# Optimization experiments

Hardware: AMD Instinct MI355X
Metric: run time of the kernel (lower is better)

Reference implementation:

```python
import jax, jax.numpy as jnp
import numpy as np

B, S, HID = 2, 2048, 2304
H, KVH, D = 8, 4, 256          # query heads, kv heads, head_dim
N_REP = H // KVH
SCALE = 256.0 ** -0.5          # query_pre_attn_scalar ** -0.5
SOFTCAP = 50.0
ROPE_THETA = 10000.0
NEG = -1e9


def setup_inputs() -> dict:
    key = jax.random.key(0)
    k1, k2, k3, k4, k5 = jax.random.split(key, 5)
    hidden_states = jax.random.normal(k1, (B, S, HID), dtype=jnp.float32)
    # RoPE cos/sin tables, shape [B, S, D]
    inv_freq = 1.0 / (ROPE_THETA ** (jnp.arange(0, D, 2, dtype=jnp.float32) / D))
    pos = jnp.arange(S, dtype=jnp.float32)
    freqs = pos[:, None] * inv_freq[None, :]            # [S, D/2]
    emb = jnp.concatenate([freqs, freqs], axis=-1)      # [S, D]
    cos = jnp.broadcast_to(jnp.cos(emb)[None], (B, S, D))
    sin = jnp.broadcast_to(jnp.sin(emb)[None], (B, S, D))
    # additive causal mask [B, 1, S, S] (sliding_window=4096 > S, so pure causal)
    idx = jnp.arange(S)
    causal = idx[None, :] <= idx[:, None]
    attention_mask = jnp.broadcast_to(
        jnp.where(causal, 0.0, NEG).astype(jnp.float32)[None, None], (B, 1, S, S))
    # projection weights (lecun-normal-ish scale), no bias (attention_bias=False)
    Wq = jax.random.normal(k2, (HID, H * D), dtype=jnp.float32) / np.sqrt(HID)
    Wk = jax.random.normal(k3, (HID, KVH * D), dtype=jnp.float32) / np.sqrt(HID)
    Wv = jax.random.normal(k4, (HID, KVH * D), dtype=jnp.float32) / np.sqrt(HID)
    Wo = jax.random.normal(k5, (H * D, HID), dtype=jnp.float32) / np.sqrt(H * D)
    return {"hidden_states": hidden_states, "cos": cos, "sin": sin,
            "attention_mask": attention_mask,
            "Wq": Wq, "Wk": Wk, "Wv": Wv, "Wo": Wo}


def _rotate_half(x):
    half = x.shape[-1] // 2
    return jnp.concatenate([-x[..., half:], x[..., :half]], axis=-1)


def reference(hidden_states, cos, sin, attention_mask, Wq, Wk, Wv, Wo):
    b, s, _ = hidden_states.shape
    q = (hidden_states @ Wq).reshape(b, s, H, D).transpose(0, 2, 1, 3)    # [B,H,S,D]
    k = (hidden_states @ Wk).reshape(b, s, KVH, D).transpose(0, 2, 1, 3)  # [B,KVH,S,D]
    v = (hidden_states @ Wv).reshape(b, s, KVH, D).transpose(0, 2, 1, 3)
    c = cos[:, None]  # [B,1,S,D] broadcast over heads (unsqueeze_dim=1)
    sn = sin[:, None]
    q = q * c + _rotate_half(q) * sn
    k = k * c + _rotate_half(k) * sn
    # GQA: repeat kv heads (interleave, matching repeat_kv tile+reshape)
    k = jnp.repeat(k, N_REP, axis=1)
    v = jnp.repeat(v, N_REP, axis=1)
    w = jnp.einsum('bhqd,bhkd->bhqk', q, k) * SCALE
    w = jnp.tanh(w / SOFTCAP) * SOFTCAP                  # logit softcapping
    w = w + attention_mask[:, :, :, :s]
    w = jax.nn.softmax(w.astype(jnp.float32), axis=-1).astype(q.dtype)
    out = jnp.einsum('bhqk,bhkd->bhqd', w, v)
    out = out.transpose(0, 2, 1, 3).reshape(b, s, H * D)
    return out @ Wo
```

## Files before the change

kernel.cpp:

```cpp
#include <hip/hip_runtime.h>

typedef unsigned short u16;
typedef __attribute__((ext_vector_type(8))) short short8;
typedef __attribute__((ext_vector_type(4))) float f32x4;
typedef __attribute__((ext_vector_type(4))) unsigned short us4;

constexpr int B_ = 2;
constexpr int H_ = 8;
constexpr int KVH_ = 4;
constexpr int S_ = 2048;
constexpr int D_ = 256;
constexpr int HID_ = 2304;
constexpr int QKVN_ = 4096;
constexpr int AON_ = 2048;

__device__ __forceinline__ float b2f(u16 u) {
  union { float f; unsigned int i; } x; x.i = ((unsigned int)u) << 16; return x.f;
}
__device__ __forceinline__ u16 f2b(float f) {
  unsigned int x = __float_as_uint(f);
  unsigned int r = (x + 0x7fffu + ((x >> 16) & 1u)) >> 16;
  return (u16)r;
}
__device__ __forceinline__ float exp2_raw(float x) {
  float r;
  asm("v_exp_f32 %0, %1" : "=v"(r) : "v"(x));
  return r;
}
__device__ __forceinline__ unsigned int cvt_pk_bf16(float lo, float hi) {
  unsigned int r;
  asm("v_cvt_pk_bf16_f32 %0, %1, %2" : "=v"(r) : "v"(lo), "v"(hi));
  return r;
}

__global__ void cast_kernel(const float* __restrict__ in, u16* __restrict__ out) {
  size_t i = ((size_t)blockIdx.x * 256 + threadIdx.x) * 4;
  float4 v = *(const float4*)(in + i);
  unsigned int lo = (unsigned int)f2b(v.x) | ((unsigned int)f2b(v.y) << 16);
  unsigned int hi = (unsigned int)f2b(v.z) | ((unsigned int)f2b(v.w) << 16);
  uint2 o; o.x = lo; o.y = hi;
  *(uint2*)(out + i) = o;
}

__global__ void transpose_cast_all(const float* __restrict__ s0, const float* __restrict__ s1,
                                   const float* __restrict__ s2, const float* __restrict__ s3,
                                   u16* __restrict__ d0, u16* __restrict__ d1,
                                   u16* __restrict__ d2, u16* __restrict__ d3) {
  __shared__ float tile[64][65];
  int which = blockIdx.z;
  const float* src; u16* dst; int R, C;
  if (which == 0)      { src = s0; dst = d0; R = 2304; C = 2048; }
  else if (which == 1) { src = s1; dst = d1; R = 2304; C = 1024; }
  else if (which == 2) { src = s2; dst = d2; R = 2304; C = 1024; }
  else                 { src = s3; dst = d3; R = 2048; C = 2304; }
  int r0 = blockIdx.y * 64, c0 = blockIdx.x * 64;
  if (r0 >= R || c0 >= C) return;
  int t = threadIdx.x;
#pragma unroll
  for (int i = 0; i < 16; ++i) {
    int e = i * 256 + t;
    int r = e >> 6, c = e & 63;
    tile[r][c] = src[(size_t)(r0 + r) * C + (c0 + c)];
  }
  __syncthreads();
#pragma unroll
  for (int i = 0; i < 8; ++i) {
    int e = i * 256 + t;
    int orow = e >> 5;
    int ocol = (e & 31) * 2;
    unsigned int w = (unsigned int)f2b(tile[ocol][orow]) |
                     ((unsigned int)f2b(tile[ocol + 1][orow]) << 16);
    *(unsigned int*)(&dst[(size_t)(c0 + orow) * R + (r0 + ocol)]) = w;
  }
}

template <int OUTF32>
__global__ __launch_bounds__(512, 2) void gemm_bt8(
    const u16* __restrict__ A, const u16* __restrict__ B, void* __restrict__ Cp,
    int M, int N, int K) {
  __shared__ u16 lds[2][2][2][8192];
  const int tid = threadIdx.x;
  const int lane = tid & 63;
  const int wave = tid >> 6;
  const int wm = wave >> 2, wn = wave & 3;
  const int quad = lane >> 4, l16 = lane & 15;
  const int m0 = blockIdx.y * 256, n0 = blockIdx.x * 256;
  const int nt = K >> 6;

  const int sub = tid >> 6;
  const int rr = (tid >> 2) & 15;
  const int cc = ((tid & 3) * 8) ^ ((rr & 8) ? 16 : 0);
  const int r_rel = (sub >> 1) * 16 + rr;
  const int ccol = (sub & 1) * 32 + cc;
  const u16* Asrc = A + (size_t)(m0 + r_rel) * K + ccol;
  const u16* Bsrc = B + (size_t)(n0 + r_rel) * K + ccol;
  const int ldsc = tid * 8;

  const int fr_off = l16 * 64 + (((quad * 8) ^ ((l16 & 8) ? 16 : 0)) << 1);

#define GL8(src, dst)                                                                  \
  __builtin_amdgcn_global_load_lds((const __attribute__((address_space(1))) void*)(src), \
                                   (__attribute__((address_space(3))) void*)(dst), 16, 0, 0)
#define STAGE_A(bf, kt, qp) {                                                          \
    const u16* _s = Asrc + (size_t)(kt) * 64;                                          \
    GL8(_s + (size_t)((qp) * 64) * K,       &lds[bf][0][0][(qp) * 4096 + ldsc]);       \
    GL8(_s + (size_t)(128 + (qp) * 64) * K, &lds[bf][0][1][(qp) * 4096 + ldsc]); }
#define STAGE_B(bf, kt, hf) {                                                          \
    const u16* _s = Bsrc + (size_t)(kt) * 64;                                          \
    GL8(_s + (size_t)((hf) * 128) * K,      &lds[bf][1][hf][ldsc]);                    \
    GL8(_s + (size_t)((hf) * 128 + 64) * K, &lds[bf][1][hf][4096 + ldsc]); }
#define LDA(bf, mi, kk) \
  (*(const short8*)((const char*)&lds[bf][0][wm][0] + (mi) * 2048 + (kk) * 1024 + fr_off))
#define LDB(bf, ni, kk) \
  (*(const short8*)((const char*)&lds[bf][1][wn >> 1][0] + ((wn & 1) * 4 + (ni)) * 2048 + (kk) * 1024 + fr_off))

  f32x4 acc[8][4] = {};
  short8 bfr[4][2], af[2][2];

  STAGE_B(0, 0, 0); STAGE_B(0, 0, 1); STAGE_A(0, 0, 0); STAGE_A(0, 0, 1);
  STAGE_B(1, 1, 0); STAGE_B(1, 1, 1); STAGE_A(1, 1, 0);
  asm volatile("s_waitcnt vmcnt(6)" ::: "memory");
  __builtin_amdgcn_s_barrier();

#define PHASE(q, STG, VMW)                                                             \
    _Pragma("unroll") for (int i = 0; i < 2; ++i)                                      \
      _Pragma("unroll") for (int kk = 0; kk < 2; ++kk) af[i][kk] = LDA(c, 2 * (q) + i, kk); \
    STG; VMW;                                                                          \
    __builtin_amdgcn_s_barrier();                                                      \
    asm volatile("s_waitcnt lgkmcnt(0)" ::: "memory");                                 \
    __builtin_amdgcn_sched_barrier(0);                                                 \
    __builtin_amdgcn_s_setprio(1);                                                     \
    _Pragma("unroll") for (int i = 0; i < 2; ++i)                                      \
      _Pragma("unroll") for (int ni = 0; ni < 4; ++ni)                                 \
        _Pragma("unroll") for (int kk = 0; kk < 2; ++kk)                               \
          acc[2 * (q) + i][ni] = __builtin_amdgcn_mfma_f32_16x16x32_bf16(              \
              af[i][kk], bfr[ni][kk], acc[2 * (q) + i][ni], 0, 0, 0);                  \
    __builtin_amdgcn_s_setprio(0);                                                     \
    __builtin_amdgcn_s_barrier();

  for (int T = 0; T < nt; ++T) {
    const int c = T & 1;
#pragma unroll
    for (int ni = 0; ni < 4; ++ni)
#pragma unroll
      for (int kk = 0; kk < 2; ++kk) bfr[ni][kk] = LDB(c, ni, kk);
    PHASE(0, if (T + 1 < nt) STAGE_A(c ^ 1, T + 1, 1), )
    PHASE(1, if (T + 2 < nt) STAGE_B(c, T + 2, 0), )
    PHASE(2, if (T + 2 < nt) STAGE_B(c, T + 2, 1), )
    PHASE(3, if (T + 2 < nt) STAGE_A(c, T + 2, 0),
          if (T + 2 >= nt) { asm volatile("s_waitcnt vmcnt(0)" ::: "memory"); }
          else             { asm volatile("s_waitcnt vmcnt(6)" ::: "memory"); })
  }
#undef PHASE
#undef LDA
#undef LDB
#undef STAGE_A
#undef STAGE_B
#undef GL8

#pragma unroll
  for (int mi = 0; mi < 8; ++mi) {
#pragma unroll
    for (int ni = 0; ni < 4; ++ni) {
#pragma unroll
      for (int r = 0; r < 4; ++r) {
        int row = m0 + wm * 128 + mi * 16 + quad * 4 + r;
        int col = n0 + wn * 64 + ni * 16 + l16;
        if (OUTF32)
          ((float*)Cp)[(size_t)row * N + col] = acc[mi][ni][r];
        else
          ((u16*)Cp)[(size_t)row * N + col] = f2b(acc[mi][ni][r]);
      }
    }
  }
}

__global__ void rope_kernel(const u16* __restrict__ qkv, const float* __restrict__ cs,
                            const float* __restrict__ sn, u16* __restrict__ Qr,
                            u16* __restrict__ Kr) {
  int t = threadIdx.x;
  int row = blockIdx.x * 8 + (t >> 5);
  int d0 = (t & 31) * 4;
  int b = row >> 11, s = row & 2047;
  const u16* qrow = qkv + (size_t)row * QKVN_;
  float4 c4 = *(const float4*)(cs + (size_t)row * D_ + d0);
  float4 s4 = *(const float4*)(sn + (size_t)row * D_ + d0);
  float c[4] = {c4.x, c4.y, c4.z, c4.w};
  float sv[4] = {s4.x, s4.y, s4.z, s4.w};
#pragma unroll
  for (int h = 0; h < H_ + KVH_; ++h) {
    const u16* src = qrow + (h < H_ ? h * D_ : 2048 + (h - H_) * D_);
    us4 lo = *(const us4*)(src + d0);
    us4 hi = *(const us4*)(src + 128 + d0);
    us4 olo, ohi;
#pragma unroll
    for (int j = 0; j < 4; ++j) {
      float xl = b2f(lo[j]), xh = b2f(hi[j]);
      olo[j] = f2b(xl * c[j] - xh * sv[j]);
      ohi[j] = f2b(xh * c[j] + xl * sv[j]);
    }
    u16* dst = (h < H_)
        ? Qr + ((size_t)(b * H_ + h) * S_ + s) * D_
        : Kr + ((size_t)(b * KVH_ + (h - H_)) * S_ + s) * D_;
    *(us4*)(dst + d0) = olo;
    *(us4*)(dst + 128 + d0) = ohi;
  }
}

__global__ void transpose_v(const u16* __restrict__ qkv, u16* __restrict__ Vt) {
  __shared__ u16 tile[64][72];
  int d0 = blockIdx.x * 64, s0 = blockIdx.y * 64, g = blockIdx.z;
  int b = g >> 2, kvh = g & 3;
  int t = threadIdx.x;
#pragma unroll
  for (int i = 0; i < 8; ++i) {
    int e = i * 256 + t;
    int r = e >> 5, c = (e & 31) * 2;
    unsigned int v = *(const unsigned int*)(&qkv[(size_t)(b * S_ + s0 + r) * QKVN_ +
                                                 3072 + kvh * D_ + d0 + c]);
    tile[r][c] = (u16)v;
    tile[r][c + 1] = (u16)(v >> 16);
  }
  __syncthreads();
#pragma unroll
  for (int i = 0; i < 8; ++i) {
    int e = i * 256 + t;
    int orow = e >> 5, ocol = (e & 31) * 2;
    unsigned int w = (unsigned int)tile[ocol][orow] |
                     ((unsigned int)tile[ocol + 1][orow] << 16);
    *(unsigned int*)(&Vt[((size_t)g * D_ + d0 + orow) * S_ + s0 + ocol]) = w;
  }
}

__global__ __launch_bounds__(256, 2) void attn_kernel(
    const u16* __restrict__ Qr, const u16* __restrict__ Kr, const u16* __restrict__ Vt,
    float* __restrict__ Op0, float* __restrict__ Op1,
    float* __restrict__ Lp0, float* __restrict__ Lp1) {
  __shared__ u16 Ks[2][32 * 256];
  __shared__ u16 Vs[2][32 * 256];
  int bx = blockIdx.x;
  int h = bx & 7;
  int u = bx >> 4;
  int sp = (bx >> 3) & 1;
  int kvh = h >> 1;
  int tid = threadIdx.x, wave = tid >> 6, lane = tid & 63;
  int quad = lane >> 4, l16 = lane & 15;
  float* Op = sp ? Op1 : Op0;
  float* Lp = sp ? Lp1 : Lp0;
  int ksrc_s[4], ksrc_c[4], vsrc_d[4], vsrc_s[4];
#pragma unroll
  for (int i = 0; i < 4; ++i) {
    int p = i * 256 + tid;
    int sK = p >> 5;
    ksrc_s[i] = sK;
    ksrc_c[i] = (p & 31) ^ ((sK & 3) | (((sK >> 3) & 1) << 2));
    vsrc_d[i] = p >> 2;
    vsrc_s[i] = (p & 3) ^ ((p >> 3) & 3);
  }
  const int kg = l16 >> 2, ka = l16 & 3;
  const int srow0 = 8 * kg + ka;
  const int ksw = ka | ((kg & 1) << 2);

  for (int part = 0; part < 2; ++part) {
    int b = part;
    int qt = (part == 0) ? u : (31 - u);
    int q0 = qt * 64;
    int beg = sp ? (qt + 1) : 0;
    int end = sp ? (2 * qt + 2) : (qt + 1);
    const u16* Qbase = Qr + ((size_t)(b * H_ + h) * S_ + q0 + wave * 16 + l16) * D_;
    short8 qf[8];
#pragma unroll
    for (int kk = 0; kk < 8; ++kk)
      qf[kk] = *(const short8*)(Qbase + kk * 32 + quad * 8);
    const u16* Kbase = Kr + (size_t)(b * KVH_ + kvh) * S_ * D_;
    const u16* Vbase = Vt + (size_t)(b * KVH_ + kvh) * D_ * S_;
    float lp = 0.f;
    f32x4 o_acc[16] = {};
    const int qq = q0 + wave * 16 + l16;

#define STAGE(KT, BUF)                                                                   \
    {                                                                                    \
      int k0s = (KT) * 32;                                                               \
      _Pragma("unroll") for (int i = 0; i < 4; ++i) {                                    \
        int p = i * 256 + tid;                                                           \
        __builtin_amdgcn_global_load_lds(                                                \
            (const __attribute__((address_space(1))) void*)(Kbase +                      \
                (size_t)(k0s + ksrc_s[i]) * D_ + ksrc_c[i] * 8),                         \
            (__attribute__((address_space(3))) void*)(&Ks[BUF][0] + p * 8), 16, 0, 0);   \
      }                                                                                  \
      _Pragma("unroll") for (int i = 0; i < 4; ++i) {                                    \
        int p = i * 256 + tid;                                                           \
        __builtin_amdgcn_global_load_lds(                                                \
            (const __attribute__((address_space(1))) void*)(Vbase +                      \
                (size_t)vsrc_d[i] * S_ + k0s + vsrc_s[i] * 8),                           \
            (__attribute__((address_space(3))) void*)(&Vs[BUF][0] + p * 8), 16, 0, 0);   \
      }                                                                                  \
    }

    STAGE(beg, 0);
    __syncthreads();
    for (int kt = beg; kt < end; ++kt) {
      int k0 = kt * 32;
      int cur = (kt - beg) & 1;
      if (kt + 1 < end) STAGE(kt + 1, cur ^ 1);
      f32x4 sacc[2] = {};
      __builtin_amdgcn_s_setprio(1);
#pragma unroll
      for (int n = 0; n < 2; ++n) {
        const u16* kb = &Ks[cur][0] + (srow0 + 4 * n) * 256;
#pragma unroll
        for (int kk = 0; kk < 8; ++kk) {
          int phys = (kk * 4 + quad) ^ ksw;
          short8 kfr = *(const short8*)(kb + phys * 8);
          sacc[n] = __builtin_amdgcn_mfma_f32_16x16x32_bf16(kfr, qf[kk], sacc[n], 0, 0, 0);
        }
      }
      __builtin_amdgcn_s_setprio(0);
      bool full = (k0 + 31 <= q0 + wave * 16);
#pragma unroll
      for (int n = 0; n < 2; ++n) {
#pragma unroll
        for (int r = 0; r < 4; ++r) {
          float E = exp2_raw(sacc[n][r] * 0.0036067376f);
          float ee = exp2_raw(__frcp_rn(E + 1.0f) * -144.2695041f);
          if (!full) {
            int key = k0 + 8 * quad + 4 * n + r;
            ee = (key <= qq) ? ee : 0.0f;
          }
          lp += ee;
          sacc[n][r] = ee;
        }
      }
      union { short8 s8; unsigned int d[4]; } pu;
      pu.d[0] = cvt_pk_bf16(sacc[0][0], sacc[0][1]);
      pu.d[1] = cvt_pk_bf16(sacc[0][2], sacc[0][3]);
      pu.d[2] = cvt_pk_bf16(sacc[1][0], sacc[1][1]);
      pu.d[3] = cvt_pk_bf16(sacc[1][2], sacc[1][3]);
      short8 pa = pu.s8;
      __builtin_amdgcn_s_setprio(1);
#pragma unroll
      for (int dt = 0; dt < 16; ++dt) {
        int d = dt * 16 + l16;
        int phys = quad ^ ((d >> 1) & 3);
        short8 vb = *(const short8*)(&Vs[cur][0] + d * 32 + phys * 8);
        o_acc[dt] = __builtin_amdgcn_mfma_f32_16x16x32_bf16(pa, vb, o_acc[dt], 0, 0, 0);
      }
      __builtin_amdgcn_s_setprio(0);
      __syncthreads();
    }
#undef STAGE
    lp += __shfl_xor(lp, 16, 64);
    lp += __shfl_xor(lp, 32, 64);
    if (lane < 16)
      Lp[((size_t)(b * H_ + h)) * S_ + q0 + wave * 16 + lane] = lp;
#pragma unroll
    for (int dt = 0; dt < 16; ++dt)
#pragma unroll
      for (int r = 0; r < 4; ++r) {
        int row = b * S_ + q0 + wave * 16 + quad * 4 + r;
        int col = h * D_ + dt * 16 + l16;
        Op[(size_t)row * AON_ + col] = o_acc[dt][r];
      }
  }
}

__global__ void combine_kernel(const float* __restrict__ Op0, const float* __restrict__ Op1,
                               const float* __restrict__ Lp0, const float* __restrict__ Lp1,
                               u16* __restrict__ Ao) {
  size_t idx = (size_t)blockIdx.x * 256 + threadIdx.x;
  size_t row = idx >> 9;
  int c4 = ((int)idx & 511) * 4;
  const float4 a = *(const float4*)(Op0 + row * AON_ + c4);
  const float4 b4 = *(const float4*)(Op1 + row * AON_ + c4);
  int b = (int)(row >> 11), s = (int)row & 2047;
  int h = c4 >> 8;
  size_t li = ((size_t)(b * H_ + h)) * S_ + s;
  float inv = 1.0f / (Lp0[li] + Lp1[li]);
  unsigned int lo = (unsigned int)f2b((a.x + b4.x) * inv) | ((unsigned int)f2b((a.y + b4.y) * inv) << 16);
  unsigned int hi = (unsigned int)f2b((a.z + b4.z) * inv) | ((unsigned int)f2b((a.w + b4.w) * inv) << 16);
  uint2 o; o.x = lo; o.y = hi;
  *(uint2*)(Ao + row * AON_ + c4) = o;
}

extern "C" void kernel_launch(void* const* d_in, const int* in_sizes, int n_in,
                              void* d_out, int out_size, void* d_ws, size_t ws_size,
                              hipStream_t stream) {
  const float* hidden = (const float*)d_in[0];
  const float* cosp = (const float*)d_in[1];
  const float* sinp = (const float*)d_in[2];
  const float* Wq = (const float*)d_in[4];
  const float* Wk = (const float*)d_in[5];
  const float* Wv = (const float*)d_in[6];
  const float* Wo = (const float*)d_in[7];

  u16* hs  = (u16*)d_ws;
  u16* WT  = hs  + (size_t)4096 * HID_;
  u16* WoT = WT  + (size_t)4096 * HID_;
  u16* qkv = WoT + (size_t)HID_ * AON_;
  u16* Qr  = qkv + (size_t)4096 * QKVN_;
  u16* Kr  = Qr  + (size_t)B_ * H_ * S_ * D_;
  u16* Vt  = Kr  + (size_t)B_ * KVH_ * S_ * D_;
  u16* Ao  = Vt  + (size_t)B_ * KVH_ * S_ * D_;
  float* Lp0 = (float*)(Ao + (size_t)4096 * AON_);
  float* Lp1 = Lp0 + (size_t)B_ * H_ * S_;
  float* Op0 = (float*)hs;
  float* Op1 = (float*)qkv;

  cast_kernel<<<9216, 256, 0, stream>>>(hidden, hs);
  transpose_cast_all<<<dim3(36, 36, 4), 256, 0, stream>>>(
      Wq, Wk, Wv, Wo, WT, WT + (size_t)2048 * HID_, WT + (size_t)3072 * HID_, WoT);
  gemm_bt8<0><<<dim3(16, 16), 512, 0, stream>>>(hs, WT, qkv, 4096, QKVN_, HID_);
  rope_kernel<<<512, 256, 0, stream>>>(qkv, cosp, sinp, Qr, Kr);
  transpose_v<<<dim3(4, 32, 8), 256, 0, stream>>>(qkv, Vt);
  attn_kernel<<<dim3(512), 256, 0, stream>>>(Qr, Kr, Vt, Op0, Op1, Lp0, Lp1);
  combine_kernel<<<16384, 256, 0, stream>>>(Op0, Op1, Lp0, Lp1, Ao);
  gemm_bt8<1><<<dim3(9, 16), 512, 0, stream>>>(Ao, WoT, d_out, 4096, HID_, 2048);
}
```

Baseline: 397.7 us.

## Merge prep and rope/V-transpose launches; use smaller-tile GEMM for output projection

Folds the hidden-state cast and the four weight transpose-casts into one launch, with a flattened grid that no longer spawns idle blocks. RoPE and the V transpose are merged into a single kernel the same way, which removes two launches. The output projection moves from the 256x256-tile GEMM (144 blocks) to a new 128x128-tile GEMM using direct global-to-LDS loads (576 blocks) to fill more CUs. The cost is a simpler GEMM with no software pipelining and more blocks that each reread the shared inputs.

```diff
diff --git a/kernel.cpp b/kernel.cpp
--- a/kernel.cpp
+++ b/kernel.cpp
@@ -33,29 +33,31 @@
   return r;
 }
 
-__global__ void cast_kernel(const float* __restrict__ in, u16* __restrict__ out) {
-  size_t i = ((size_t)blockIdx.x * 256 + threadIdx.x) * 4;
-  float4 v = *(const float4*)(in + i);
-  unsigned int lo = (unsigned int)f2b(v.x) | ((unsigned int)f2b(v.y) << 16);
-  unsigned int hi = (unsigned int)f2b(v.z) | ((unsigned int)f2b(v.w) << 16);
-  uint2 o; o.x = lo; o.y = hi;
-  *(uint2*)(out + i) = o;
-}
-
-__global__ void transpose_cast_all(const float* __restrict__ s0, const float* __restrict__ s1,
-                                   const float* __restrict__ s2, const float* __restrict__ s3,
-                                   u16* __restrict__ d0, u16* __restrict__ d1,
-                                   u16* __restrict__ d2, u16* __restrict__ d3) {
+__global__ void prep_kernel(const float* __restrict__ hidden,
+                            const float* __restrict__ s0, const float* __restrict__ s1,
+                            const float* __restrict__ s2, const float* __restrict__ s3,
+                            u16* __restrict__ hsOut,
+                            u16* __restrict__ d0, u16* __restrict__ d1,
+                            u16* __restrict__ d2, u16* __restrict__ d3) {
   __shared__ float tile[64][65];
-  int which = blockIdx.z;
-  const float* src; u16* dst; int R, C;
-  if (which == 0)      { src = s0; dst = d0; R = 2304; C = 2048; }
-  else if (which == 1) { src = s1; dst = d1; R = 2304; C = 1024; }
-  else if (which == 2) { src = s2; dst = d2; R = 2304; C = 1024; }
-  else                 { src = s3; dst = d3; R = 2048; C = 2304; }
-  int r0 = blockIdx.y * 64, c0 = blockIdx.x * 64;
-  if (r0 >= R || c0 >= C) return;
+  int bx = blockIdx.x;
   int t = threadIdx.x;
+  if (bx < 9216) {
+    size_t i = ((size_t)bx * 256 + t) * 4;
+    float4 v = *(const float4*)(hidden + i);
+    unsigned int lo = (unsigned int)f2b(v.x) | ((unsigned int)f2b(v.y) << 16);
+    unsigned int hi = (unsigned int)f2b(v.z) | ((unsigned int)f2b(v.w) << 16);
+    uint2 o; o.x = lo; o.y = hi;
+    *(uint2*)(hsOut + i) = o;
+    return;
+  }
+  int tt = bx - 9216;
+  const float* src; u16* dst; int R, C, cx, cy;
+  if (tt < 1152)              { src = s0; dst = d0; R = 2304; C = 2048; cx = tt & 31; cy = tt >> 5; }
+  else if ((tt -= 1152) < 576){ src = s1; dst = d1; R = 2304; C = 1024; cx = tt & 15; cy = tt >> 4; }
+  else if ((tt -= 576) < 576) { src = s2; dst = d2; R = 2304; C = 1024; cx = tt & 15; cy = tt >> 4; }
+  else { tt -= 576;             src = s3; dst = d3; R = 2048; C = 2304; cx = tt % 36; cy = tt / 36; }
+  int r0 = cy * 64, c0 = cx * 64;
 #pragma unroll
   for (int i = 0; i < 16; ++i) {
     int e = i * 256 + t;
@@ -175,43 +177,108 @@
   }
 }
 
-__global__ void rope_kernel(const u16* __restrict__ qkv, const float* __restrict__ cs,
-                            const float* __restrict__ sn, u16* __restrict__ Qr,
-                            u16* __restrict__ Kr) {
+template <int OUTF32>
+__global__ __launch_bounds__(256, 2) void gemm_bt(
+    const u16* __restrict__ A, const u16* __restrict__ B, void* __restrict__ Cp,
+    int M, int N, int K) {
+  __shared__ u16 As[128 * 32];
+  __shared__ u16 Bs[128 * 32];
+  int m0 = blockIdx.y * 128, n0 = blockIdx.x * 128;
+  int tid = threadIdx.x;
+  int lane = tid & 63, wave = tid >> 6;
+  int wy = wave >> 1, wx = wave & 1;
+  int quad = lane >> 4, l16 = lane & 15;
+  f32x4 acc[4][4] = {};
+  for (int k0 = 0; k0 < K; k0 += 32) {
+#pragma unroll
+    for (int i = 0; i < 2; ++i) {
+      int chunk = i * 256 + tid;
+      int row = chunk >> 2, col = (chunk & 3) << 3;
+      __builtin_amdgcn_global_load_lds(
+          (const __attribute__((address_space(1))) void*)(A + (size_t)(m0 + row) * K + k0 + col),
+          (__attribute__((address_space(3))) void*)(As + chunk * 8), 16, 0, 0);
+    }
+#pragma unroll
+    for (int i = 0; i < 2; ++i) {
+      int chunk = i * 256 + tid;
+      int row = chunk >> 2, col = (chunk & 3) << 3;
+      __builtin_amdgcn_global_load_lds(
+          (const __attribute__((address_space(1))) void*)(B + (size_t)(n0 + row) * K + k0 + col),
+          (__attribute__((address_space(3))) void*)(Bs + chunk * 8), 16, 0, 0);
+    }
+    __syncthreads();
+    short8 af[4], bf[4];
+#pragma unroll
+    for (int mi = 0; mi < 4; ++mi)
+      af[mi] = *(const short8*)(As + (wy * 64 + mi * 16 + l16) * 32 + quad * 8);
+#pragma unroll
+    for (int ni = 0; ni < 4; ++ni)
+      bf[ni] = *(const short8*)(Bs + (wx * 64 + ni * 16 + l16) * 32 + quad * 8);
+#pragma unroll
+    for (int mi = 0; mi < 4; ++mi)
+#pragma unroll
+      for (int ni = 0; ni < 4; ++ni)
+        acc[mi][ni] = __builtin_amdgcn_mfma_f32_16x16x32_bf16(af[mi], bf[ni], acc[mi][ni], 0, 0, 0);
+    __syncthreads();
+  }
+#pragma unroll
+  for (int mi = 0; mi < 4; ++mi) {
+#pragma unroll
+    for (int ni = 0; ni < 4; ++ni) {
+#pragma unroll
+      for (int r = 0; r < 4; ++r) {
+        int row = m0 + wy * 64 + mi * 16 + quad * 4 + r;
+        int col = n0 + wx * 64 + ni * 16 + l16;
+        if (OUTF32)
+          ((float*)Cp)[(size_t)row * N + col] = acc[mi][ni][r];
+        else
+          ((u16*)Cp)[(size_t)row * N + col] = f2b(acc[mi][ni][r]);
+      }
+    }
+  }
+}
+
+__global__ void rope_tv_kernel(const u16* __restrict__ qkv, const float* __restrict__ cs,
+                               const float* __restrict__ sn, u16* __restrict__ Qr,
+                               u16* __restrict__ Kr, u16* __restrict__ Vt) {
+  __shared__ u16 tile[64][72];
+  int bx = blockIdx.x;
   int t = threadIdx.x;
-  int row = blockIdx.x * 8 + (t >> 5);
-  int d0 = (t & 31) * 4;
-  int b = row >> 11, s = row & 2047;
-  const u16* qrow = qkv + (size_t)row * QKVN_;
-  float4 c4 = *(const float4*)(cs + (size_t)row * D_ + d0);
-  float4 s4 = *(const float4*)(sn + (size_t)row * D_ + d0);
-  float c[4] = {c4.x, c4.y, c4.z, c4.w};
-  float sv[4] = {s4.x, s4.y, s4.z, s4.w};
-#pragma unroll
-  for (int h = 0; h < H_ + KVH_; ++h) {
-    const u16* src = qrow + (h < H_ ? h * D_ : 2048 + (h - H_) * D_);
-    us4 lo = *(const us4*)(src + d0);
-    us4 hi = *(const us4*)(src + 128 + d0);
-    us4 olo, ohi;
-#pragma unroll
-    for (int j = 0; j < 4; ++j) {
-      float xl = b2f(lo[j]), xh = b2f(hi[j]);
-      olo[j] = f2b(xl * c[j] - xh * sv[j]);
-      ohi[j] = f2b(xh * c[j] + xl * sv[j]);
-    }
-    u16* dst = (h < H_)
-        ? Qr + ((size_t)(b * H_ + h) * S_ + s) * D_
-        : Kr + ((size_t)(b * KVH_ + (h - H_)) * S_ + s) * D_;
-    *(us4*)(dst + d0) = olo;
-    *(us4*)(dst + 128 + d0) = ohi;
-  }
-}
-
-__global__ void transpose_v(const u16* __restrict__ qkv, u16* __restrict__ Vt) {
-  __shared__ u16 tile[64][72];
-  int d0 = blockIdx.x * 64, s0 = blockIdx.y * 64, g = blockIdx.z;
+  if (bx < 512) {
+    int row = bx * 8 + (t >> 5);
+    int d0 = (t & 31) * 4;
+    int b = row >> 11, s = row & 2047;
+    const u16* qrow = qkv + (size_t)row * QKVN_;
+    float4 c4 = *(const float4*)(cs + (size_t)row * D_ + d0);
+    float4 s4 = *(const float4*)(sn + (size_t)row * D_ + d0);
+    float c[4] = {c4.x, c4.y, c4.z, c4.w};
+    float sv[4] = {s4.x, s4.y, s4.z, s4.w};
+#pragma unroll
+    for (int h = 0; h < H_ + KVH_; ++h) {
+      const u16* src = qrow + (h < H_ ? h * D_ : 2048 + (h - H_) * D_);
+      us4 lo = *(const us4*)(src + d0);
+      us4 hi = *(const us4*)(src + 128 + d0);
+      us4 olo, ohi;
+#pragma unroll
+      for (int j = 0; j < 4; ++j) {
+        float xl = b2f(lo[j]), xh = b2f(hi[j]);
+        olo[j] = f2b(xl * c[j] - xh * sv[j]);
+        ohi[j] = f2b(xh * c[j] + xl * sv[j]);
+      }
+      u16* dst = (h < H_)
+          ? Qr + ((size_t)(b * H_ + h) * S_ + s) * D_
+          : Kr + ((size_t)(b * KVH_ + (h - H_)) * S_ + s) * D_;
+      *(us4*)(dst + d0) = olo;
+      *(us4*)(dst + 128 + d0) = ohi;
+    }
+    return;
+  }
+  int tt = bx - 512;
+  int g = tt >> 7;
+  int rem = tt & 127;
+  int s0 = (rem >> 2) * 64;
+  int d0 = (rem & 3) * 64;
   int b = g >> 2, kvh = g & 3;
-  int t = threadIdx.x;
 #pragma unroll
   for (int i = 0; i < 8; ++i) {
     int e = i * 256 + t;
@@ -406,13 +473,12 @@
   float* Op0 = (float*)hs;
   float* Op1 = (float*)qkv;
 
-  cast_kernel<<<9216, 256, 0, stream>>>(hidden, hs);
-  transpose_cast_all<<<dim3(36, 36, 4), 256, 0, stream>>>(
-      Wq, Wk, Wv, Wo, WT, WT + (size_t)2048 * HID_, WT + (size_t)3072 * HID_, WoT);
+  prep_kernel<<<12672, 256, 0, stream>>>(
+      hidden, Wq, Wk, Wv, Wo, hs,
+      WT, WT + (size_t)2048 * HID_, WT + (size_t)3072 * HID_, WoT);
   gemm_bt8<0><<<dim3(16, 16), 512, 0, stream>>>(hs, WT, qkv, 4096, QKVN_, HID_);
-  rope_kernel<<<512, 256, 0, stream>>>(qkv, cosp, sinp, Qr, Kr);
-  transpose_v<<<dim3(4, 32, 8), 256, 0, stream>>>(qkv, Vt);
+  rope_tv_kernel<<<1536, 256, 0, stream>>>(qkv, cosp, sinp, Qr, Kr, Vt);
   attn_kernel<<<dim3(512), 256, 0, stream>>>(Qr, Kr, Vt, Op0, Op1, Lp0, Lp1);
   combine_kernel<<<16384, 256, 0, stream>>>(Op0, Op1, Lp0, Lp1, Ao);
-  gemm_bt8<1><<<dim3(9, 16), 512, 0, stream>>>(Ao, WoT, d_out, 4096, HID_, 2048);
-}
+  gemm_bt<1><<<dim3(18, 32), 256, 0, stream>>>(Ao, WoT, d_out, 4096, HID_, 2048);
+}
```

Result: no change. 390.1 us (-1.9%).
